# Performance work log

Measured on AMD Instinct MI355X. Metric: run time of the kernel, lower is better.

Reference implementation:

```python
import jax, jax.numpy as jnp
import numpy as np

N_NODES = 100000
N_EDGES = 1600000
IN_C = 256
H1 = 128
H2 = 64
OUT_C = 64


def setup_inputs() -> dict:
    key = jax.random.key(0)
    ks = jax.random.split(key, 8)
    x = jax.random.normal(ks[0], (N_NODES, IN_C), dtype=jnp.float32)
    edge_src = jax.random.randint(ks[1], (N_EDGES,), 0, N_NODES, dtype=jnp.int32)
    edge_dst = jax.random.randint(ks[2], (N_EDGES,), 0, N_NODES, dtype=jnp.int32)
    edge_weight = jax.random.uniform(ks[3], (N_EDGES,), dtype=jnp.float32)
    W1 = jax.random.normal(ks[4], (IN_C, H1), dtype=jnp.float32) / np.sqrt(IN_C)
    b1 = jnp.zeros((H1,), dtype=jnp.float32)
    W2 = jax.random.normal(ks[5], (H1, H2), dtype=jnp.float32) / np.sqrt(H1)
    b2 = jnp.zeros((H2,), dtype=jnp.float32)
    W3 = jax.random.normal(ks[6], (H2, OUT_C), dtype=jnp.float32) / np.sqrt(H2)
    b3 = jnp.zeros((OUT_C,), dtype=jnp.float32)
    return dict(x=x, edge_src=edge_src, edge_dst=edge_dst, edge_weight=edge_weight,
                W1=W1, b1=b1, W2=W2, b2=b2, W3=W3, b3=b3)


def _gcn_layer(h, W, b, src, dst, ew):
    # GraphConvolution: out = adj @ (h @ W) + b, adj given as weighted edge list
    support = h @ W                      # [N, d_out] dense GEMM
    msg = support[src] * ew[:, None]     # [E, d_out] gather (irregular access)
    agg = jax.ops.segment_sum(msg, dst, num_segments=N_NODES)  # SpMM scatter-add
    return agg + b


def reference(x, edge_src, edge_dst, edge_weight, W1, b1, W2, b2, W3, b3):
    # Eval-mode forward: dropout is identity (training=False)
    h = jax.nn.relu(_gcn_layer(x, W1, b1, edge_src, edge_dst, edge_weight))
    h = jax.nn.relu(_gcn_layer(h, W2, b2, edge_src, edge_dst, edge_weight))
    out = _gcn_layer(h, W3, b3, edge_src, edge_dst, edge_weight)
    return out
```

## Files before the change

kernel.cpp:

```cpp
#include <hip/hip_runtime.h>
#include <hip/hip_bf16.h>


#define EPB 8192

__device__ __forceinline__ unsigned short f2bf(float f) {
    unsigned int u = __float_as_uint(f);
    unsigned int r = (u + 0x7fffu + ((u >> 16) & 1u)) >> 16;
    return (unsigned short)r;
}

using frag_ab = __attribute__((ext_vector_type(8))) short;
using frag_cd = __attribute__((ext_vector_type(4))) float;

template <int BN>
__global__ __launch_bounds__(256) void mfma_gemm_kernel(
    const float* __restrict__ A, const unsigned short* __restrict__ WT,
    unsigned short* __restrict__ C, int M, int K)
{
    constexpr int BM = 128, BK = 64;
    constexpr int LDA = BK + 8;
    __shared__ unsigned short As[BM * LDA];
    __shared__ unsigned short Bs[BN * LDA];

    const int tid = threadIdx.x;
    const int wave = tid >> 6;
    const int lane = tid & 63;
    const int quad = lane >> 4;
    const int l16 = lane & 15;
    const int m0 = blockIdx.x * BM;

    frag_cd acc[2][BN / 16];
#pragma unroll
    for (int rt = 0; rt < 2; ++rt)
#pragma unroll
        for (int f = 0; f < BN / 16; ++f) acc[rt][f] = (frag_cd){0.f, 0.f, 0.f, 0.f};

    for (int k0 = 0; k0 < K; k0 += BK) {
#pragma unroll
        for (int i = 0; i < 8; ++i) {
            const int linear = (i * 256 + tid) * 4;
            const int r = linear >> 6;
            const int c = linear & 63;
            const int row = m0 + r;
            float4 v = make_float4(0.f, 0.f, 0.f, 0.f);
            if (row < M) v = *(const float4*)&A[(size_t)row * K + k0 + c];
            ushort4 u;
            u.x = f2bf(v.x); u.y = f2bf(v.y); u.z = f2bf(v.z); u.w = f2bf(v.w);
            *(ushort4*)&As[r * LDA + c] = u;
        }
#pragma unroll
        for (int i = 0; i < BN / 32; ++i) {
            const int linear = (i * 256 + tid) * 8;
            const int n = linear >> 6;
            const int c = linear & 63;
            const uint4 u = *(const uint4*)&WT[(size_t)n * K + k0 + c];
            *(uint4*)&Bs[n * LDA + c] = u;
        }
        __syncthreads();

#pragma unroll
        for (int ks = 0; ks < 2; ++ks) {
            const int kk = ks * 32 + quad * 8;
            const frag_ab a0 = *(const frag_ab*)&As[(wave * 32 + l16) * LDA + kk];
            const frag_ab a1 = *(const frag_ab*)&As[(wave * 32 + 16 + l16) * LDA + kk];
#pragma unroll
            for (int f = 0; f < BN / 16; ++f) {
                const frag_ab b = *(const frag_ab*)&Bs[(f * 16 + l16) * LDA + kk];
                acc[0][f] = __builtin_amdgcn_mfma_f32_16x16x32_bf16(a0, b, acc[0][f], 0, 0, 0);
                acc[1][f] = __builtin_amdgcn_mfma_f32_16x16x32_bf16(a1, b, acc[1][f], 0, 0, 0);
            }
        }
        __syncthreads();
    }

#pragma unroll
    for (int rt = 0; rt < 2; ++rt)
#pragma unroll
        for (int f = 0; f < BN / 16; ++f)
#pragma unroll
            for (int r = 0; r < 4; ++r) {
                const int row = m0 + wave * 32 + rt * 16 + quad * 4 + r;
                if (row < M) C[(size_t)row * BN + f * 16 + l16] = f2bf(acc[rt][f][r]);
            }
}

__global__ __launch_bounds__(256) void wt_kernel(
    const float* __restrict__ W1, const float* __restrict__ W2, const float* __restrict__ W3,
    unsigned short* __restrict__ WT1, unsigned short* __restrict__ WT2, unsigned short* __restrict__ WT3)
{
    const int i = blockIdx.x * 256 + threadIdx.x;
    const float* W; unsigned short* WT; int K, N, j;
    if (i < 32768)      { W = W1; WT = WT1; K = 256; N = 128; j = i; }
    else if (i < 40960) { W = W2; WT = WT2; K = 128; N = 64;  j = i - 32768; }
    else if (i < 45056) { W = W3; WT = WT3; K = 64;  N = 64;  j = i - 40960; }
    else return;
    const int n = j / K, k = j % K;
    WT[j] = f2bf(W[k * N + n]);
}

__global__ __launch_bounds__(256) void count_kernel(
    const int* __restrict__ dst, int* __restrict__ cmat, int E, int nblk, int nbuck)
{
    __shared__ int hist[1600];
    for (int i = threadIdx.x; i < nbuck; i += 256) hist[i] = 0;
    __syncthreads();
    const int base = blockIdx.x * EPB;
    const int end = min(base + EPB, E);
    for (int e = base + threadIdx.x; e < end; e += 256)
        atomicAdd(&hist[dst[e] >> 6], 1);
    __syncthreads();
    for (int i = threadIdx.x; i < nbuck; i += 256)
        cmat[(size_t)i * nblk + blockIdx.x] = hist[i];
}

__global__ __launch_bounds__(256) void scanA_kernel(
    int* __restrict__ data, int* __restrict__ psum, int L)
{
    __shared__ int tmp[256];
    const int b0 = blockIdx.x * 1024 + threadIdx.x * 4;
    int v[4] = {0, 0, 0, 0};
    if (b0 + 3 < L) { const int4 t = *(const int4*)&data[b0]; v[0]=t.x; v[1]=t.y; v[2]=t.z; v[3]=t.w; }
    else { for (int i = 0; i < 4; ++i) if (b0 + i < L) v[i] = data[b0 + i]; }
    const int s = v[0] + v[1] + v[2] + v[3];
    tmp[threadIdx.x] = s;
    __syncthreads();
#pragma unroll
    for (int d = 1; d < 256; d <<= 1) {
        const int t = (threadIdx.x >= d) ? tmp[threadIdx.x - d] : 0;
        __syncthreads();
        tmp[threadIdx.x] += t;
        __syncthreads();
    }
    int run = tmp[threadIdx.x] - s;
    int o[4];
#pragma unroll
    for (int i = 0; i < 4; ++i) { o[i] = run; run += v[i]; }
    if (b0 + 3 < L) { *(int4*)&data[b0] = make_int4(o[0], o[1], o[2], o[3]); }
    else { for (int i = 0; i < 4; ++i) if (b0 + i < L) data[b0 + i] = o[i]; }
    if (threadIdx.x == 255) psum[blockIdx.x] = tmp[255];
}

__global__ __launch_bounds__(1024) void scanB_kernel(int* __restrict__ psum, int nb)
{
    __shared__ int tmp[1024];
    const int v = ((int)threadIdx.x < nb) ? psum[threadIdx.x] : 0;
    tmp[threadIdx.x] = v;
    __syncthreads();
#pragma unroll
    for (int d = 1; d < 1024; d <<= 1) {
        const int t = ((int)threadIdx.x >= d) ? tmp[threadIdx.x - d] : 0;
        __syncthreads();
        tmp[threadIdx.x] += t;
        __syncthreads();
    }
    if ((int)threadIdx.x < nb) psum[threadIdx.x] = tmp[threadIdx.x] - v;
}

__global__ __launch_bounds__(256) void scanC_kernel(
    int* __restrict__ data, const int* __restrict__ psum, int L)
{
    const int i = blockIdx.x * 256 + threadIdx.x;
    if (i < L) data[i] += psum[i >> 10];
}

__global__ __launch_bounds__(256) void place_kernel(
    const int* __restrict__ src, const int* __restrict__ dst, const float* __restrict__ ew,
    const int* __restrict__ cmat, uint2* __restrict__ ebuck, int E, int nblk, int nbuck)
{
    __shared__ int cursor[1600];
    const int k = blockIdx.x;
    for (int i = threadIdx.x; i < nbuck; i += 256)
        cursor[i] = cmat[(size_t)i * nblk + k];
    __syncthreads();
    const int base = k * EPB;
    const int end = min(base + EPB, E);
    for (int e = base + threadIdx.x; e < end; e += 256) {
        const int d = dst[e];
        const int b = d >> 6;
        const int pos = atomicAdd(&cursor[b], 1);
        ebuck[pos] = make_uint2(((unsigned)src[e] << 6) | (unsigned)(d & 63),
                                __float_as_uint(ew[e]));
    }
}

__global__ __launch_bounds__(256) void sort2_kernel(
    const uint2* __restrict__ ebuck, const int* __restrict__ cmat,
    int* __restrict__ offs, uint2* __restrict__ ecsr,
    int N, int nblk, int nbuck, int E)
{
    __shared__ int cnt[64];
    __shared__ int cur[64];
    const int b = blockIdx.x;
    const int node0 = b << 6;
    const int nn = min(64, N - node0);
    const int j0 = cmat[(size_t)b * nblk];
    const int j1 = (b + 1 < nbuck) ? cmat[(size_t)(b + 1) * nblk] : E;

    if (threadIdx.x < 64) cnt[threadIdx.x] = 0;
    __syncthreads();
    for (int j = j0 + (int)threadIdx.x; j < j1; j += 256)
        atomicAdd(&cnt[ebuck[j].x & 63u], 1);
    __syncthreads();

    if (threadIdx.x < 64) {
        const int myv = cnt[threadIdx.x];
        int v = myv;
#pragma unroll
        for (int d = 1; d < 64; d <<= 1) {
            const int t = __shfl_up(v, d, 64);
            if ((int)threadIdx.x >= d) v += t;
        }
        const int base = j0 + v - myv;
        cur[threadIdx.x] = base;
        if ((int)threadIdx.x < nn) offs[node0 + threadIdx.x] = base;
        if (threadIdx.x == 0 && b == nbuck - 1) offs[N] = E;
    }
    __syncthreads();

    for (int j = j0 + (int)threadIdx.x; j < j1; j += 256) {
        const uint2 ed = ebuck[j];
        const int pos = atomicAdd(&cur[ed.x & 63u], 1);
        ecsr[pos] = make_uint2(ed.x >> 6, ed.y);
    }
}

template <int D, int LOGT, bool RELU>
__global__ __launch_bounds__(256) void gather_agg_kernel(
    const unsigned short* __restrict__ S, const int* __restrict__ offs,
    const uint2* __restrict__ ecsr,
    const float* __restrict__ bias, float* __restrict__ out, int N)
{
    const int TPN = 1 << LOGT;
    const int gid = blockIdx.x * 256 + threadIdx.x;
    const int node = gid >> LOGT;
    if (node >= N) return;
    const int lane = gid & (TPN - 1);
    const int c8 = lane << 3;

    const int j0 = offs[node];
    const int j1 = offs[node + 1];

    float acc[8];
#pragma unroll
    for (int c = 0; c < 8; ++c) acc[c] = 0.f;

    int jb = j0;
    for (; jb + TPN <= j1; jb += TPN) {
        const uint2 p = ecsr[jb + lane];
        const int myc = (int)p.x;
        const float myw = __uint_as_float(p.y);
#pragma unroll
        for (int t = 0; t < TPN; ++t) {
            const int s = __shfl(myc, t, TPN);
            const float w = __shfl(myw, t, TPN);
            const uint4 v = *(const uint4*)&S[(size_t)s * D + c8];
#pragma unroll
            for (int q = 0; q < 4; ++q) {
                const unsigned int u = (&v.x)[q];
                acc[q * 2 + 0] += w * __uint_as_float(u << 16);
                acc[q * 2 + 1] += w * __uint_as_float(u & 0xffff0000u);
            }
        }
    }
    if (jb < j1) {
        const int j = jb + lane;
        int myc = 0;
        float myw = 0.f;
        if (j < j1) {
            const uint2 p = ecsr[j];
            myc = (int)p.x;
            myw = __uint_as_float(p.y);
        }
        const int cnt = j1 - jb;
        for (int t = 0; t < cnt; ++t) {
            const int s = __shfl(myc, t, TPN);
            const float w = __shfl(myw, t, TPN);
            const uint4 v = *(const uint4*)&S[(size_t)s * D + c8];
#pragma unroll
            for (int q = 0; q < 4; ++q) {
                const unsigned int u = (&v.x)[q];
                acc[q * 2 + 0] += w * __uint_as_float(u << 16);
                acc[q * 2 + 1] += w * __uint_as_float(u & 0xffff0000u);
            }
        }
    }

#pragma unroll
    for (int c = 0; c < 8; ++c) {
        float v = acc[c] + bias[c8 + c];
        if (RELU) v = fmaxf(v, 0.f);
        acc[c] = v;
    }
    float4* op = (float4*)&out[(size_t)node * D + c8];
    op[0] = make_float4(acc[0], acc[1], acc[2], acc[3]);
    op[1] = make_float4(acc[4], acc[5], acc[6], acc[7]);
}

extern "C" void kernel_launch(void* const* d_in, const int* in_sizes, int n_in,
                              void* d_out, int out_size, void* d_ws, size_t ws_size,
                              hipStream_t stream)
{
    const float* x    = (const float*)d_in[0];
    const int*   esrc = (const int*)  d_in[1];
    const int*   edst = (const int*)  d_in[2];
    const float* ew   = (const float*)d_in[3];
    const float* W1   = (const float*)d_in[4];
    const float* b1   = (const float*)d_in[5];
    const float* W2   = (const float*)d_in[6];
    const float* b2   = (const float*)d_in[7];
    const float* W3   = (const float*)d_in[8];
    const float* b3   = (const float*)d_in[9];

    const int N = in_sizes[0] / 256;
    const int E = in_sizes[1];

    const int nbuck = (N + 63) >> 6;
    const int nblk = (E + EPB - 1) / EPB;
    const int L = nbuck * nblk;

    unsigned short* Sb = (unsigned short*)d_ws;
    float* H   = (float*)(Sb + (size_t)N * 128);
    unsigned short* WT1 = (unsigned short*)(H + (size_t)N * 128);
    unsigned short* WT2 = WT1 + 256 * 128;
    unsigned short* WT3 = WT2 + 128 * 64;
    uint2* ebuck = (uint2*)(WT3 + 64 * 64);
    uint2* ecsr  = ebuck + E;
    int* offs   = (int*)(ecsr + E);
    int* cmat   = offs + N + 4;
    int* psum   = cmat + ((L + 3) & ~3);
    float* out  = (float*)d_out;

    const dim3 blk(256);
    const int mblocks = (N + 127) / 128;

    wt_kernel<<<(45056 + 255) / 256, blk, 0, stream>>>(W1, W2, W3, WT1, WT2, WT3);
    count_kernel<<<nblk, blk, 0, stream>>>(edst, cmat, E, nblk, nbuck);
    scanA_kernel<<<(L + 1023) / 1024, blk, 0, stream>>>(cmat, psum, L);
    scanB_kernel<<<1, 1024, 0, stream>>>(psum, (L + 1023) / 1024);
    scanC_kernel<<<(L + 255) / 256, blk, 0, stream>>>(cmat, psum, L);
    place_kernel<<<nblk, blk, 0, stream>>>(esrc, edst, ew, cmat, ebuck, E, nblk, nbuck);
    sort2_kernel<<<nbuck, blk, 0, stream>>>(ebuck, cmat, offs, ecsr, N, nblk, nbuck, E);

    mfma_gemm_kernel<128><<<mblocks, blk, 0, stream>>>(x, WT1, Sb, N, 256);
    gather_agg_kernel<128, 4, true><<<((N * 16) + 255) / 256, blk, 0, stream>>>(
        Sb, offs, ecsr, b1, H, N);

    mfma_gemm_kernel<64><<<mblocks, blk, 0, stream>>>(H, WT2, Sb, N, 128);
    gather_agg_kernel<64, 3, true><<<((N * 8) + 255) / 256, blk, 0, stream>>>(
        Sb, offs, ecsr, b2, H, N);

    mfma_gemm_kernel<64><<<mblocks, blk, 0, stream>>>(H, WT3, Sb, N, 64);
    gather_agg_kernel<64, 3, false><<<((N * 8) + 255) / 256, blk, 0, stream>>>(
        Sb, offs, ecsr, b3, out, N);
}
```

Baseline: 463.7 us.

## Store intermediate activations in bf16, prefetch edge chunks, use nontemporal memory ops

The intermediate hidden activations H are now written as bf16 by the aggregation kernels and read directly as bf16 by the next GEMM. This halves their write and read traffic and removes the fp32-to-bf16 conversion in the GEMM load stage. The aggregation loop also software-prefetches the next chunk of CSR edges, and several loads and stores are switched to nontemporal hints. GEMM inputs were already rounded to bf16, so numerics should barely change, but nontemporal loads of ecsr and H could lose useful cache reuse.

```diff
diff --git a/kernel.cpp b/kernel.cpp
--- a/kernel.cpp
+++ b/kernel.cpp
@@ -3,6 +3,10 @@
 
 
 #define EPB 8192
+
+typedef unsigned int u32x4 __attribute__((ext_vector_type(4)));
+typedef unsigned int u32x2 __attribute__((ext_vector_type(2)));
+typedef float        f32x4 __attribute__((ext_vector_type(4)));
 
 __device__ __forceinline__ unsigned short f2bf(float f) {
     unsigned int u = __float_as_uint(f);
@@ -13,9 +17,9 @@
 using frag_ab = __attribute__((ext_vector_type(8))) short;
 using frag_cd = __attribute__((ext_vector_type(4))) float;
 
-template <int BN>
+template <int BN, bool ABF16>
 __global__ __launch_bounds__(256) void mfma_gemm_kernel(
-    const float* __restrict__ A, const unsigned short* __restrict__ WT,
+    const void* __restrict__ Av, const unsigned short* __restrict__ WT,
     unsigned short* __restrict__ C, int M, int K)
 {
     constexpr int BM = 128, BK = 64;
@@ -37,25 +41,40 @@
         for (int f = 0; f < BN / 16; ++f) acc[rt][f] = (frag_cd){0.f, 0.f, 0.f, 0.f};
 
     for (int k0 = 0; k0 < K; k0 += BK) {
-#pragma unroll
-        for (int i = 0; i < 8; ++i) {
-            const int linear = (i * 256 + tid) * 4;
-            const int r = linear >> 6;
-            const int c = linear & 63;
-            const int row = m0 + r;
-            float4 v = make_float4(0.f, 0.f, 0.f, 0.f);
-            if (row < M) v = *(const float4*)&A[(size_t)row * K + k0 + c];
-            ushort4 u;
-            u.x = f2bf(v.x); u.y = f2bf(v.y); u.z = f2bf(v.z); u.w = f2bf(v.w);
-            *(ushort4*)&As[r * LDA + c] = u;
+        if constexpr (!ABF16) {
+            const float* A = (const float*)Av;
+#pragma unroll
+            for (int i = 0; i < 8; ++i) {
+                const int linear = (i * 256 + tid) * 4;
+                const int r = linear >> 6;
+                const int c = linear & 63;
+                const int row = m0 + r;
+                f32x4 v = (f32x4){0.f, 0.f, 0.f, 0.f};
+                if (row < M) v = __builtin_nontemporal_load((const f32x4*)&A[(size_t)row * K + k0 + c]);
+                ushort4 u;
+                u.x = f2bf(v.x); u.y = f2bf(v.y); u.z = f2bf(v.z); u.w = f2bf(v.w);
+                *(ushort4*)&As[r * LDA + c] = u;
+            }
+        } else {
+            const unsigned short* A = (const unsigned short*)Av;
+#pragma unroll
+            for (int i = 0; i < 4; ++i) {
+                const int linear = (i * 256 + tid) * 8;
+                const int r = linear >> 6;
+                const int c = linear & 63;
+                const int row = m0 + r;
+                u32x4 u = (u32x4){0u, 0u, 0u, 0u};
+                if (row < M) u = __builtin_nontemporal_load((const u32x4*)&A[(size_t)row * K + k0 + c]);
+                *(u32x4*)&As[r * LDA + c] = u;
+            }
         }
 #pragma unroll
         for (int i = 0; i < BN / 32; ++i) {
             const int linear = (i * 256 + tid) * 8;
             const int n = linear >> 6;
             const int c = linear & 63;
-            const uint4 u = *(const uint4*)&WT[(size_t)n * K + k0 + c];
-            *(uint4*)&Bs[n * LDA + c] = u;
+            const u32x4 u = *(const u32x4*)&WT[(size_t)n * K + k0 + c];
+            *(u32x4*)&Bs[n * LDA + c] = u;
         }
         __syncthreads();
 
@@ -225,13 +244,13 @@
     }
 }
 
-template <int D, int LOGT, bool RELU>
+template <int D, int LOGT, bool RELU, typename OUT_T>
 __global__ __launch_bounds__(256) void gather_agg_kernel(
     const unsigned short* __restrict__ S, const int* __restrict__ offs,
     const uint2* __restrict__ ecsr,
-    const float* __restrict__ bias, float* __restrict__ out, int N)
-{
-    const int TPN = 1 << LOGT;
+    const float* __restrict__ bias, OUT_T* __restrict__ out, int N)
+{
+    constexpr int TPN = 1 << LOGT;
     const int gid = blockIdx.x * 256 + threadIdx.x;
     const int node = gid >> LOGT;
     if (node >= N) return;
@@ -246,8 +265,14 @@
     for (int c = 0; c < 8; ++c) acc[c] = 0.f;
 
     int jb = j0;
-    for (; jb + TPN <= j1; jb += TPN) {
-        const uint2 p = ecsr[jb + lane];
+    u32x2 p = (u32x2){0u, 0u};
+    if (jb + lane < j1) p = __builtin_nontemporal_load((const u32x2*)&ecsr[jb + lane]);
+
+    const int nfull = (j1 - j0) >> LOGT;
+    for (int ch = 0; ch < nfull; ++ch) {
+        const int jn = jb + TPN;
+        u32x2 pn = (u32x2){0u, 0u};
+        if (jn + lane < j1) pn = __builtin_nontemporal_load((const u32x2*)&ecsr[jn + lane]);
         const int myc = (int)p.x;
         const float myw = __uint_as_float(p.y);
 #pragma unroll
@@ -262,17 +287,12 @@
                 acc[q * 2 + 1] += w * __uint_as_float(u & 0xffff0000u);
             }
         }
-    }
-    if (jb < j1) {
-        const int j = jb + lane;
-        int myc = 0;
-        float myw = 0.f;
-        if (j < j1) {
-            const uint2 p = ecsr[j];
-            myc = (int)p.x;
-            myw = __uint_as_float(p.y);
-        }
+        p = pn; jb = jn;
+    }
+    {
         const int cnt = j1 - jb;
+        const int myc = (int)p.x;
+        const float myw = __uint_as_float(p.y);
         for (int t = 0; t < cnt; ++t) {
             const int s = __shfl(myc, t, TPN);
             const float w = __shfl(myw, t, TPN);
@@ -292,9 +312,18 @@
         if (RELU) v = fmaxf(v, 0.f);
         acc[c] = v;
     }
-    float4* op = (float4*)&out[(size_t)node * D + c8];
-    op[0] = make_float4(acc[0], acc[1], acc[2], acc[3]);
-    op[1] = make_float4(acc[4], acc[5], acc[6], acc[7]);
+    if constexpr (sizeof(OUT_T) == 2) {
+        u32x4 u;
+        u.x = ((unsigned)f2bf(acc[1]) << 16) | (unsigned)f2bf(acc[0]);
+        u.y = ((unsigned)f2bf(acc[3]) << 16) | (unsigned)f2bf(acc[2]);
+        u.z = ((unsigned)f2bf(acc[5]) << 16) | (unsigned)f2bf(acc[4]);
+        u.w = ((unsigned)f2bf(acc[7]) << 16) | (unsigned)f2bf(acc[6]);
+        __builtin_nontemporal_store(u, (u32x4*)&((unsigned short*)out)[(size_t)node * D + c8]);
+    } else {
+        float* op = (float*)out + (size_t)node * D + c8;
+        __builtin_nontemporal_store((f32x4){acc[0], acc[1], acc[2], acc[3]}, (f32x4*)op);
+        __builtin_nontemporal_store((f32x4){acc[4], acc[5], acc[6], acc[7]}, (f32x4*)op + 1);
+    }
 }
 
 extern "C" void kernel_launch(void* const* d_in, const int* in_sizes, int n_in,
@@ -320,8 +349,8 @@
     const int L = nbuck * nblk;
 
     unsigned short* Sb = (unsigned short*)d_ws;
-    float* H   = (float*)(Sb + (size_t)N * 128);
-    unsigned short* WT1 = (unsigned short*)(H + (size_t)N * 128);
+    unsigned short* Hb = Sb + (size_t)N * 128;
+    unsigned short* WT1 = Hb + (size_t)N * 128;
     unsigned short* WT2 = WT1 + 256 * 128;
     unsigned short* WT3 = WT2 + 128 * 64;
     uint2* ebuck = (uint2*)(WT3 + 64 * 64);
@@ -342,15 +371,15 @@
     place_kernel<<<nblk, blk, 0, stream>>>(esrc, edst, ew, cmat, ebuck, E, nblk, nbuck);
     sort2_kernel<<<nbuck, blk, 0, stream>>>(ebuck, cmat, offs, ecsr, N, nblk, nbuck, E);
 
-    mfma_gemm_kernel<128><<<mblocks, blk, 0, stream>>>(x, WT1, Sb, N, 256);
-    gather_agg_kernel<128, 4, true><<<((N * 16) + 255) / 256, blk, 0, stream>>>(
-        Sb, offs, ecsr, b1, H, N);
-
-    mfma_gemm_kernel<64><<<mblocks, blk, 0, stream>>>(H, WT2, Sb, N, 128);
-    gather_agg_kernel<64, 3, true><<<((N * 8) + 255) / 256, blk, 0, stream>>>(
-        Sb, offs, ecsr, b2, H, N);
-
-    mfma_gemm_kernel<64><<<mblocks, blk, 0, stream>>>(H, WT3, Sb, N, 64);
-    gather_agg_kernel<64, 3, false><<<((N * 8) + 255) / 256, blk, 0, stream>>>(
+    mfma_gemm_kernel<128, false><<<mblocks, blk, 0, stream>>>(x, WT1, Sb, N, 256);
+    gather_agg_kernel<128, 4, true, unsigned short><<<((N * 16) + 255) / 256, blk, 0, stream>>>(
+        Sb, offs, ecsr, b1, Hb, N);
+
+    mfma_gemm_kernel<64, true><<<mblocks, blk, 0, stream>>>(Hb, WT2, Sb, N, 128);
+    gather_agg_kernel<64, 3, true, unsigned short><<<((N * 8) + 255) / 256, blk, 0, stream>>>(
+        Sb, offs, ecsr, b2, Hb, N);
+
+    mfma_gemm_kernel<64, true><<<mblocks, blk, 0, stream>>>(Hb, WT3, Sb, N, 64);
+    gather_agg_kernel<64, 3, false, float><<<((N * 8) + 255) / 256, blk, 0, stream>>>(
         Sb, offs, ecsr, b3, out, N);
 }
```

New measurement: 474.2 us. 1.02x slower.
